# Kernel tuning notes

Measured on AMD Instinct MI355X. Metric: run time of the kernel, lower is better.

Reference implementation:

```python
import jax, jax.numpy as jnp
import numpy as np

H, B, N, F, O = 8, 2, 2048, 256, 64
NEG_INF = jnp.float32(-9e15)


def _xavier(key, shape):
    fan_in, fan_out = shape[-2], shape[-1]
    limit = np.sqrt(6.0 / (fan_in + fan_out))
    return jax.random.uniform(key, shape, dtype=jnp.float32, minval=-limit, maxval=limit)


def setup_inputs() -> dict:
    key = jax.random.key(0)
    k1, k2, k3, k4, k5 = jax.random.split(key, 5)
    x = jax.random.normal(k1, (B, N, F), dtype=jnp.float32)
    adj = (jax.random.uniform(k2, (B, N, N)) < 0.05).astype(jnp.float32)
    adj = jnp.maximum(adj, jnp.eye(N, dtype=jnp.float32))
    W = _xavier(k3, (H, F, O))           # self.linear
    a_src = _xavier(k4, (H, O, 1))       # attention_vect_src
    a_dst = _xavier(k5, (H, O, 1))       # attention_vect_dst
    return {"x": x, "adj": adj, "W": W, "a_src": a_src, "a_dst": a_dst}


def reference(x, adj, W, a_src, a_dst):
    # h: [H, B, N, O]  (per-head linear projection)
    h = jnp.einsum('bnf,hfo->hbno', x, W)
    # additive attention scalars per node: [H, B, N]
    s_src = jnp.einsum('hbno,ho->hbn', h, a_src[..., 0])
    s_dst = jnp.einsum('hbno,ho->hbn', h, a_dst[..., 0])
    # score[h,b,i,j] = s_dst[i] + s_src[j]  -> [H, B, N, N]
    score = s_dst[..., :, None] + s_src[..., None, :]
    score = jax.nn.leaky_relu(score, negative_slope=0.2)
    score = jnp.where(adj > 0, score, NEG_INF)
    att = jax.nn.softmax(score, axis=-1) * adj  # dropout = identity (eval)
    # weighted aggregation of neighbor features: [H, B, N, O]
    out = jnp.einsum('hbij,hbjo->hbio', att, h)
    # concat heads along feature dim (head order preserved): [B, N, H*O]
    out = jnp.transpose(out, (1, 2, 0, 3)).reshape(B, N, H * O)
    return jax.nn.relu(out)
```

## Files before the change

kernel.cpp:

```cpp
#include <hip/hip_runtime.h>

#define H_ 8
#define B_ 2
#define N_ 2048
#define F_ 256
#define O_ 64
#define CAP 256
#define KPAD 264

typedef unsigned short u16;
typedef unsigned int   u32;
typedef __attribute__((ext_vector_type(8))) short bf16x8;
typedef __attribute__((ext_vector_type(4))) float f32x4;

__device__ __forceinline__ float us2f(u16 u) {
    union { u32 i; float f; } c; c.i = ((u32)u) << 16; return c.f;
}
__device__ __forceinline__ u16 f2us(float f) {
    union { float f; u32 i; } c; c.f = f; return (u16)(c.i >> 16);
}

__global__ void detect_kernel(const uint4* __restrict__ adj_v, int* __restrict__ flag) {
    __shared__ int found;
    if (threadIdx.x == 0) found = 0;
    __syncthreads();
#pragma unroll
    for (int i = 0; i < 16; ++i) {
        uint4 v = adj_v[threadIdx.x * 16 + i];
        u32 w[4] = {v.x, v.y, v.z, v.w};
        for (int q = 0; q < 4; ++q)
            if (w[q] == 0x00003F80u || w[q] == 0x3F803F80u) found = 1;
    }
    __syncthreads();
    if (threadIdx.x == 0) flag[0] = found;
}

__global__ __launch_bounds__(256) void proj_kernel(const void* __restrict__ x,
                                                   const void* __restrict__ W,
                                                   const void* __restrict__ a_src,
                                                   const void* __restrict__ a_dst,
                                                   const int* __restrict__ flag,
                                                   float* __restrict__ hT,
                                                   float* __restrict__ sTsrc,
                                                   float* __restrict__ sTdst) {
    __shared__ alignas(16) u16 xs[64 * KPAD];
    __shared__ alignas(16) u16 wt[64 * KPAD];

    int bf   = flag[0];
    int bx   = blockIdx.x;
    int h    = bx & 7;
    int bn0  = (bx >> 3) * 64;
    int tid  = threadIdx.x;
    int wave = tid >> 6;
    int lane = tid & 63;

    if (bf) {
        const u16* xg = (const u16*)x;
#pragma unroll
        for (int p = 0; p < 8; ++p) {
            int r = wave * 16 + p * 2 + (lane >> 5);
            int c = (lane & 31) * 8;
            *(uint4*)(xs + r * KPAD + c) = *(const uint4*)(xg + (size_t)(bn0 + r) * F_ + c);
        }
    } else {
        const float* xg = (const float*)x;
#pragma unroll
        for (int p = 0; p < 8; ++p) {
            int r = wave * 16 + p * 2 + (lane >> 5);
            int c = (lane & 31) * 8;
            for (int q = 0; q < 8; ++q)
                xs[r * KPAD + c + q] = f2us(xg[(size_t)(bn0 + r) * F_ + c + q]);
        }
    }
    {
        int o  = tid & 63;
        int fq = tid >> 6;
        if (bf) {
            const u16* wg = (const u16*)W + (size_t)h * F_ * O_;
            for (int i = 0; i < 64; ++i) {
                int f = fq * 64 + i;
                wt[o * KPAD + f] = wg[(size_t)f * O_ + o];
            }
        } else {
            const float* wg = (const float*)W + (size_t)h * F_ * O_;
            for (int i = 0; i < 64; ++i) {
                int f = fq * 64 + i;
                wt[o * KPAD + f] = f2us(wg[(size_t)f * O_ + o]);
            }
        }
    }
    __syncthreads();

    int m_l  = lane & 15;
    int quad = lane >> 4;
    int mrow = wave * 16 + m_l;

    f32x4 acc[4] = {{0,0,0,0},{0,0,0,0},{0,0,0,0},{0,0,0,0}};
#pragma unroll
    for (int ks = 0; ks < 8; ++ks) {
        int kofs = ks * 32 + quad * 8;
        bf16x8 afrag = *(const bf16x8*)(xs + mrow * KPAD + kofs);
#pragma unroll
        for (int nt = 0; nt < 4; ++nt) {
            bf16x8 bfrag = *(const bf16x8*)(wt + (nt * 16 + m_l) * KPAD + kofs);
            acc[nt] = __builtin_amdgcn_mfma_f32_16x16x32_bf16(afrag, bfrag, acc[nt], 0, 0, 0);
        }
    }

    float asv[4], adv[4];
#pragma unroll
    for (int nt = 0; nt < 4; ++nt) {
        int o = nt * 16 + m_l;
        if (bf) {
            asv[nt] = us2f(((const u16*)a_src)[h * 64 + o]);
            adv[nt] = us2f(((const u16*)a_dst)[h * 64 + o]);
        } else {
            asv[nt] = ((const float*)a_src)[h * 64 + o];
            adv[nt] = ((const float*)a_dst)[h * 64 + o];
        }
    }
    float vs[4] = {0,0,0,0}, vd[4] = {0,0,0,0};
#pragma unroll
    for (int nt = 0; nt < 4; ++nt)
#pragma unroll
        for (int r = 0; r < 4; ++r) {
            float hv = acc[nt][r];
            int row = wave * 16 + quad * 4 + r;
            hT[(size_t)(bn0 + row) * (H_ * O_) + h * O_ + nt * 16 + m_l] = hv;
            vs[r] = fmaf(hv, asv[nt], vs[r]);
            vd[r] = fmaf(hv, adv[nt], vd[r]);
        }
#pragma unroll
    for (int r = 0; r < 4; ++r)
#pragma unroll
        for (int off = 1; off < 16; off <<= 1) {
            vs[r] += __shfl_xor(vs[r], off);
            vd[r] += __shfl_xor(vd[r], off);
        }
    if (m_l == 0) {
#pragma unroll
        for (int r = 0; r < 4; ++r) {
            int row = wave * 16 + quad * 4 + r;
            sTsrc[(size_t)(bn0 + row) * H_ + h] = vs[r];
            sTdst[(size_t)(bn0 + row) * H_ + h] = vd[r];
        }
    }
}

__global__ void csr_kernel(const void* __restrict__ adj,
                           const int* __restrict__ flag,
                           int* __restrict__ cnt,
                           u16* __restrict__ nidx) {
    __shared__ int scnt;
    __shared__ u16 sidx[CAP];
    int row = blockIdx.x;
    int tid = threadIdx.x;
    if (tid == 0) scnt = 0;
    __syncthreads();

    if (flag[0]) {
        const u16* arow = (const u16*)adj + (size_t)row * N_;
        uint4 v = *(const uint4*)(arow + tid * 8);
        u32 w[4] = {v.x, v.y, v.z, v.w};
        int j0 = tid * 8;
#pragma unroll
        for (int q = 0; q < 4; ++q) {
            if (w[q] & 0xFFFFu) { int p = atomicAdd(&scnt, 1); if (p < CAP) sidx[p] = (u16)(j0 + 2 * q); }
            if (w[q] >> 16)     { int p = atomicAdd(&scnt, 1); if (p < CAP) sidx[p] = (u16)(j0 + 2 * q + 1); }
        }
    } else {
        const float* arow = (const float*)adj + (size_t)row * N_;
        for (int j = tid; j < N_; j += 256) {
            if (arow[j] > 0.f) { int p = atomicAdd(&scnt, 1); if (p < CAP) sidx[p] = (u16)j; }
        }
    }
    __syncthreads();
    int m = scnt < CAP ? scnt : CAP;
    if (tid == 0) cnt[row] = m;
    for (int k = tid; k < m; k += 256) nidx[(size_t)row * CAP + k] = sidx[k];
}

__global__ void GATLayer_88072599371930_kernel(const float* __restrict__ hT,
                                               const float* __restrict__ sTsrc,
                                               const float* __restrict__ sTdst,
                                               const int* __restrict__ cnt,
                                               const u16* __restrict__ nidx,
                                               float* __restrict__ out) {
    __shared__ u16   sj[CAP];
    __shared__ float se[CAP * H_];
    __shared__ float mh[H_];
    __shared__ float rzh[H_];
    __shared__ float sdl[H_];
    __shared__ float sred[128 * 4];

    int bi  = blockIdx.x;
    int tid = threadIdx.x;
    int n   = cnt[bi];
    int base = bi & ~(N_ - 1);

    if (tid < 8) sdl[tid] = sTdst[(size_t)bi * H_ + tid];
    if (tid < n) sj[tid] = nidx[(size_t)bi * CAP + tid];
    __syncthreads();

    if (n <= 0) {
        out[(size_t)bi * 512 + tid] = 999.0f;
        out[(size_t)bi * 512 + 256 + tid] = 999.0f;
        return;
    }

    int tot = n * H_;
    for (int idx = tid; idx < tot; idx += 256) {
        int k  = idx >> 3;
        int hh = idx & 7;
        int j  = sj[k];
        float v = sdl[hh] + sTsrc[(size_t)(base + j) * H_ + hh];
        v = v > 0.f ? v : 0.2f * v;
        se[idx] = v;
    }
    __syncthreads();

    if (tid < 64) {
        int hh = tid >> 3, kk = tid & 7;
        float lm = -3.4e38f;
        for (int k = kk; k < n; k += 8) lm = fmaxf(lm, se[k * 8 + hh]);
#pragma unroll
        for (int mm = 1; mm < 8; mm <<= 1) lm = fmaxf(lm, __shfl_xor(lm, mm));
        if (kk == 0) mh[hh] = lm;
    }
    __syncthreads();

    for (int idx = tid; idx < tot; idx += 256) {
        int hh = idx & 7;
        se[idx] = __expf(se[idx] - mh[hh]);
    }
    __syncthreads();

    if (tid < 64) {
        int hh = tid >> 3, kk = tid & 7;
        float ls = 0.f;
        for (int k = kk; k < n; k += 8) ls += se[k * 8 + hh];
#pragma unroll
        for (int mm = 1; mm < 8; mm <<= 1) ls += __shfl_xor(ls, mm);
        if (kk == 0) rzh[hh] = 1.f / ls;
    }
    __syncthreads();

    int slot = tid >> 7;
    int hh   = (tid >> 4) & 7;
    int oq   = tid & 15;
    const float* hb = hT + (size_t)base * 512;
    float a0 = 0.f, a1 = 0.f, a2 = 0.f, a3 = 0.f;
    for (int k = slot; k < n; k += 2) {
        int j   = sj[k];
        float w = se[k * 8 + hh];
        const float4 hv = *(const float4*)(hb + (size_t)j * 512 + hh * 64 + oq * 4);
        a0 = fmaf(w, hv.x, a0);
        a1 = fmaf(w, hv.y, a1);
        a2 = fmaf(w, hv.z, a2);
        a3 = fmaf(w, hv.w, a3);
    }
    if (slot == 1) {
        float4 t; t.x = a0; t.y = a1; t.z = a2; t.w = a3;
        ((float4*)sred)[tid - 128] = t;
    }
    __syncthreads();
    if (slot == 0) {
        float4 p = ((float4*)sred)[tid];
        float rz = rzh[hh];
        float4 r;
        r.x = fmaxf((a0 + p.x) * rz, 0.f);
        r.y = fmaxf((a1 + p.y) * rz, 0.f);
        r.z = fmaxf((a2 + p.z) * rz, 0.f);
        r.w = fmaxf((a3 + p.w) * rz, 0.f);
        *(float4*)(out + (size_t)bi * 512 + tid * 4) = r;
    }
}

extern "C" void kernel_launch(void* const* d_in, const int* in_sizes, int n_in,
                              void* d_out, int out_size, void* d_ws, size_t ws_size,
                              hipStream_t stream) {
    const void *x = 0, *adj = 0, *W = 0, *a_src = 0, *a_dst = 0;
    for (int i = 0; i < n_in; ++i) {
        long sz = in_sizes[i];
        if (sz == (long)B_ * N_ * F_)      x = d_in[i];
        else if (sz == (long)B_ * N_ * N_) adj = d_in[i];
        else if (sz == (long)H_ * F_ * O_) W = d_in[i];
        else if (sz == (long)H_ * O_) { if (!a_src) a_src = d_in[i]; else a_dst = d_in[i]; }
    }
    if (!x)     x     = d_in[0];
    if (!adj)   adj   = d_in[1];
    if (!W)     W     = d_in[2];
    if (!a_src) a_src = d_in[3];
    if (!a_dst) a_dst = d_in[4];

    float* out = (float*)d_out;

    char* ws = (char*)d_ws;
    size_t off = 0;
    int*   flag  = (int*)(ws + off);   off += 256;
    float* hT    = (float*)(ws + off); off += (size_t)B_ * N_ * H_ * O_ * 4;
    float* sTsrc = (float*)(ws + off); off += (size_t)B_ * N_ * H_ * 4;
    float* sTdst = (float*)(ws + off); off += (size_t)B_ * N_ * H_ * 4;
    int*   cnt   = (int*)(ws + off);   off += (size_t)B_ * N_ * 4;
    u16*   nidx  = (u16*)(ws + off);   off += (size_t)B_ * N_ * CAP * 2;

    detect_kernel<<<dim3(1), dim3(256), 0, stream>>>((const uint4*)adj, flag);
    proj_kernel<<<dim3((N_ * B_ / 64) * H_), dim3(256), 0, stream>>>(
        x, W, a_src, a_dst, flag, hT, sTsrc, sTdst);
    csr_kernel<<<dim3(B_ * N_), dim3(256), 0, stream>>>(adj, flag, cnt, nidx);
    GATLayer_88072599371930_kernel<<<dim3(B_ * N_), dim3(256), 0, stream>>>(
        hT, sTsrc, sTdst, cnt, nidx, out);
}
```

Before: 150.5 us.

## Fuse CSR build into attention kernel, pre-transpose W, stream x fragments directly

Removes the separate CSR kernel and its global cnt/nidx round trip by building each row's neighbour list in shared memory inside the attention kernel. W is transposed and converted to bf16 once in a small new kernel, so each projection block only does vectorised copies of it into LDS. Projection A fragments are read straight from global memory instead of being staged through LDS, which cuts shared memory use. The aggregation loop is unrolled four ways to keep more gathers in flight, and bf16 conversion now rounds to nearest instead of truncating.

```diff
diff --git a/kernel.cpp b/kernel.cpp
--- a/kernel.cpp
+++ b/kernel.cpp
@@ -16,8 +16,10 @@
 __device__ __forceinline__ float us2f(u16 u) {
     union { u32 i; float f; } c; c.i = ((u32)u) << 16; return c.f;
 }
-__device__ __forceinline__ u16 f2us(float f) {
-    union { float f; u32 i; } c; c.f = f; return (u16)(c.i >> 16);
+__device__ __forceinline__ u16 f2us_rn(float f) {
+    union { float f; u32 i; } c; c.f = f;
+    u32 r = c.i + 0x7FFFu + ((c.i >> 16) & 1u);
+    return (u16)(r >> 16);
 }
 
 __global__ void detect_kernel(const uint4* __restrict__ adj_v, int* __restrict__ flag) {
@@ -35,15 +37,36 @@
     if (threadIdx.x == 0) flag[0] = found;
 }
 
+__global__ void wt_kernel(const void* __restrict__ W,
+                          const int* __restrict__ flag,
+                          u16* __restrict__ Wt) {
+    int h  = blockIdx.x;
+    int o  = threadIdx.x & 63;
+    int fq = threadIdx.x >> 6;
+    u16* dst = Wt + (size_t)h * O_ * F_ + (size_t)o * F_;
+    if (flag[0]) {
+        const u16* wg = (const u16*)W + (size_t)h * F_ * O_;
+        for (int i = 0; i < 64; ++i) {
+            int f = fq * 64 + i;
+            dst[f] = wg[(size_t)f * O_ + o];
+        }
+    } else {
+        const float* wg = (const float*)W + (size_t)h * F_ * O_;
+        for (int i = 0; i < 64; ++i) {
+            int f = fq * 64 + i;
+            dst[f] = f2us_rn(wg[(size_t)f * O_ + o]);
+        }
+    }
+}
+
 __global__ __launch_bounds__(256) void proj_kernel(const void* __restrict__ x,
-                                                   const void* __restrict__ W,
+                                                   const u16* __restrict__ Wt,
                                                    const void* __restrict__ a_src,
                                                    const void* __restrict__ a_dst,
                                                    const int* __restrict__ flag,
                                                    float* __restrict__ hT,
                                                    float* __restrict__ sTsrc,
                                                    float* __restrict__ sTdst) {
-    __shared__ alignas(16) u16 xs[64 * KPAD];
     __shared__ alignas(16) u16 wt[64 * KPAD];
 
     int bf   = flag[0];
@@ -54,52 +77,33 @@
     int wave = tid >> 6;
     int lane = tid & 63;
 
-    if (bf) {
-        const u16* xg = (const u16*)x;
-#pragma unroll
-        for (int p = 0; p < 8; ++p) {
-            int r = wave * 16 + p * 2 + (lane >> 5);
-            int c = (lane & 31) * 8;
-            *(uint4*)(xs + r * KPAD + c) = *(const uint4*)(xg + (size_t)(bn0 + r) * F_ + c);
-        }
-    } else {
-        const float* xg = (const float*)x;
-#pragma unroll
-        for (int p = 0; p < 8; ++p) {
-            int r = wave * 16 + p * 2 + (lane >> 5);
-            int c = (lane & 31) * 8;
-            for (int q = 0; q < 8; ++q)
-                xs[r * KPAD + c + q] = f2us(xg[(size_t)(bn0 + r) * F_ + c + q]);
-        }
-    }
     {
-        int o  = tid & 63;
-        int fq = tid >> 6;
-        if (bf) {
-            const u16* wg = (const u16*)W + (size_t)h * F_ * O_;
-            for (int i = 0; i < 64; ++i) {
-                int f = fq * 64 + i;
-                wt[o * KPAD + f] = wg[(size_t)f * O_ + o];
-            }
-        } else {
-            const float* wg = (const float*)W + (size_t)h * F_ * O_;
-            for (int i = 0; i < 64; ++i) {
-                int f = fq * 64 + i;
-                wt[o * KPAD + f] = f2us(wg[(size_t)f * O_ + o]);
-            }
-        }
+        int o    = tid >> 2;
+        int part = tid & 3;
+        const u16* src = Wt + (size_t)h * O_ * F_ + (size_t)o * F_ + part * 64;
+        u16* dst = wt + o * KPAD + part * 64;
+#pragma unroll
+        for (int i = 0; i < 8; ++i)
+            *(uint4*)(dst + i * 8) = *(const uint4*)(src + i * 8);
     }
     __syncthreads();
 
     int m_l  = lane & 15;
     int quad = lane >> 4;
-    int mrow = wave * 16 + m_l;
+    int mrow = bn0 + wave * 16 + m_l;
 
     f32x4 acc[4] = {{0,0,0,0},{0,0,0,0},{0,0,0,0},{0,0,0,0}};
 #pragma unroll
     for (int ks = 0; ks < 8; ++ks) {
         int kofs = ks * 32 + quad * 8;
-        bf16x8 afrag = *(const bf16x8*)(xs + mrow * KPAD + kofs);
+        bf16x8 afrag;
+        if (bf) {
+            afrag = *(const bf16x8*)((const u16*)x + (size_t)mrow * F_ + kofs);
+        } else {
+            const float* xr = (const float*)x + (size_t)mrow * F_ + kofs;
+#pragma unroll
+            for (int q = 0; q < 8; ++q) afrag[q] = (short)f2us_rn(xr[q]);
+        }
 #pragma unroll
         for (int nt = 0; nt < 4; ++nt) {
             bf16x8 bfrag = *(const bf16x8*)(wt + (nt * 16 + m_l) * KPAD + kofs);
@@ -147,45 +151,13 @@
     }
 }
 
-__global__ void csr_kernel(const void* __restrict__ adj,
-                           const int* __restrict__ flag,
-                           int* __restrict__ cnt,
-                           u16* __restrict__ nidx) {
-    __shared__ int scnt;
-    __shared__ u16 sidx[CAP];
-    int row = blockIdx.x;
-    int tid = threadIdx.x;
-    if (tid == 0) scnt = 0;
-    __syncthreads();
-
-    if (flag[0]) {
-        const u16* arow = (const u16*)adj + (size_t)row * N_;
-        uint4 v = *(const uint4*)(arow + tid * 8);
-        u32 w[4] = {v.x, v.y, v.z, v.w};
-        int j0 = tid * 8;
-#pragma unroll
-        for (int q = 0; q < 4; ++q) {
-            if (w[q] & 0xFFFFu) { int p = atomicAdd(&scnt, 1); if (p < CAP) sidx[p] = (u16)(j0 + 2 * q); }
-            if (w[q] >> 16)     { int p = atomicAdd(&scnt, 1); if (p < CAP) sidx[p] = (u16)(j0 + 2 * q + 1); }
-        }
-    } else {
-        const float* arow = (const float*)adj + (size_t)row * N_;
-        for (int j = tid; j < N_; j += 256) {
-            if (arow[j] > 0.f) { int p = atomicAdd(&scnt, 1); if (p < CAP) sidx[p] = (u16)j; }
-        }
-    }
-    __syncthreads();
-    int m = scnt < CAP ? scnt : CAP;
-    if (tid == 0) cnt[row] = m;
-    for (int k = tid; k < m; k += 256) nidx[(size_t)row * CAP + k] = sidx[k];
-}
-
 __global__ void GATLayer_88072599371930_kernel(const float* __restrict__ hT,
                                                const float* __restrict__ sTsrc,
                                                const float* __restrict__ sTdst,
-                                               const int* __restrict__ cnt,
-                                               const u16* __restrict__ nidx,
+                                               const void* __restrict__ adj,
+                                               const int* __restrict__ flag,
                                                float* __restrict__ out) {
+    __shared__ int   scnt;
     __shared__ u16   sj[CAP];
     __shared__ float se[CAP * H_];
     __shared__ float mh[H_];
@@ -193,14 +165,32 @@
     __shared__ float sdl[H_];
     __shared__ float sred[128 * 4];
 
-    int bi  = blockIdx.x;
-    int tid = threadIdx.x;
-    int n   = cnt[bi];
+    int bi   = blockIdx.x;
+    int tid  = threadIdx.x;
     int base = bi & ~(N_ - 1);
 
+    if (tid == 0) scnt = 0;
     if (tid < 8) sdl[tid] = sTdst[(size_t)bi * H_ + tid];
-    if (tid < n) sj[tid] = nidx[(size_t)bi * CAP + tid];
-    __syncthreads();
+    __syncthreads();
+
+    if (flag[0]) {
+        const u16* arow = (const u16*)adj + (size_t)bi * N_;
+        uint4 v = *(const uint4*)(arow + tid * 8);
+        u32 w[4] = {v.x, v.y, v.z, v.w};
+        int j0 = tid * 8;
+#pragma unroll
+        for (int q = 0; q < 4; ++q) {
+            if (w[q] & 0xFFFFu) { int p = atomicAdd(&scnt, 1); if (p < CAP) sj[p] = (u16)(j0 + 2 * q); }
+            if (w[q] >> 16)     { int p = atomicAdd(&scnt, 1); if (p < CAP) sj[p] = (u16)(j0 + 2 * q + 1); }
+        }
+    } else {
+        const float* arow = (const float*)adj + (size_t)bi * N_;
+        for (int j = tid; j < N_; j += 256) {
+            if (arow[j] > 0.f) { int p = atomicAdd(&scnt, 1); if (p < CAP) sj[p] = (u16)j; }
+        }
+    }
+    __syncthreads();
+    int n = scnt < CAP ? scnt : CAP;
 
     if (n <= 0) {
         out[(size_t)bi * 512 + tid] = 999.0f;
@@ -248,16 +238,27 @@
     int slot = tid >> 7;
     int hh   = (tid >> 4) & 7;
     int oq   = tid & 15;
-    const float* hb = hT + (size_t)base * 512;
+    const float* hb = hT + (size_t)base * 512 + hh * 64 + oq * 4;
     float a0 = 0.f, a1 = 0.f, a2 = 0.f, a3 = 0.f;
-    for (int k = slot; k < n; k += 2) {
-        int j   = sj[k];
+    int k = slot;
+    for (; k + 6 < n; k += 8) {
+        int   j0 = sj[k],     j1 = sj[k + 2], j2 = sj[k + 4], j3 = sj[k + 6];
+        float w0 = se[k * 8 + hh],       w1 = se[(k + 2) * 8 + hh];
+        float w2 = se[(k + 4) * 8 + hh], w3 = se[(k + 6) * 8 + hh];
+        float4 v0 = *(const float4*)(hb + (size_t)j0 * 512);
+        float4 v1 = *(const float4*)(hb + (size_t)j1 * 512);
+        float4 v2 = *(const float4*)(hb + (size_t)j2 * 512);
+        float4 v3 = *(const float4*)(hb + (size_t)j3 * 512);
+        a0 = fmaf(w0, v0.x, a0); a1 = fmaf(w0, v0.y, a1); a2 = fmaf(w0, v0.z, a2); a3 = fmaf(w0, v0.w, a3);
+        a0 = fmaf(w1, v1.x, a0); a1 = fmaf(w1, v1.y, a1); a2 = fmaf(w1, v1.z, a2); a3 = fmaf(w1, v1.w, a3);
+        a0 = fmaf(w2, v2.x, a0); a1 = fmaf(w2, v2.y, a1); a2 = fmaf(w2, v2.z, a2); a3 = fmaf(w2, v2.w, a3);
+        a0 = fmaf(w3, v3.x, a0); a1 = fmaf(w3, v3.y, a1); a2 = fmaf(w3, v3.z, a2); a3 = fmaf(w3, v3.w, a3);
+    }
+    for (; k < n; k += 2) {
+        int   j = sj[k];
         float w = se[k * 8 + hh];
-        const float4 hv = *(const float4*)(hb + (size_t)j * 512 + hh * 64 + oq * 4);
-        a0 = fmaf(w, hv.x, a0);
-        a1 = fmaf(w, hv.y, a1);
-        a2 = fmaf(w, hv.z, a2);
-        a3 = fmaf(w, hv.w, a3);
+        float4 v = *(const float4*)(hb + (size_t)j * 512);
+        a0 = fmaf(w, v.x, a0); a1 = fmaf(w, v.y, a1); a2 = fmaf(w, v.z, a2); a3 = fmaf(w, v.w, a3);
     }
     if (slot == 1) {
         float4 t; t.x = a0; t.y = a1; t.z = a2; t.w = a3;
@@ -301,13 +302,12 @@
     float* hT    = (float*)(ws + off); off += (size_t)B_ * N_ * H_ * O_ * 4;
     float* sTsrc = (float*)(ws + off); off += (size_t)B_ * N_ * H_ * 4;
     float* sTdst = (float*)(ws + off); off += (size_t)B_ * N_ * H_ * 4;
-    int*   cnt   = (int*)(ws + off);   off += (size_t)B_ * N_ * 4;
-    u16*   nidx  = (u16*)(ws + off);   off += (size_t)B_ * N_ * CAP * 2;
+    u16*   Wt    = (u16*)(ws + off);   off += (size_t)H_ * O_ * F_ * 2;
 
     detect_kernel<<<dim3(1), dim3(256), 0, stream>>>((const uint4*)adj, flag);
+    wt_kernel<<<dim3(H_), dim3(256), 0, stream>>>(W, flag, Wt);
     proj_kernel<<<dim3((N_ * B_ / 64) * H_), dim3(256), 0, stream>>>(
-        x, W, a_src, a_dst, flag, hT, sTsrc, sTdst);
-    csr_kernel<<<dim3(B_ * N_), dim3(256), 0, stream>>>(adj, flag, cnt, nidx);
+        x, Wt, a_src, a_dst, flag, hT, sTsrc, sTdst);
     GATLayer_88072599371930_kernel<<<dim3(B_ * N_), dim3(256), 0, stream>>>(
-        hT, sTsrc, sTdst, cnt, nidx, out);
-}
+        hT, sTsrc, sTdst, adj, flag, out);
+}
```

Result: no change. 147.7 us (-1.8%).
